# Optimization experiments

Hardware: AMD Instinct MI355X
Metric: run time of the kernel (lower is better)

Reference implementation:

```python
import jax, jax.numpy as jnp
import numpy as np

CUTOFF = 10.0
K = 32            # max_num_neighbors
NUM_GRAPHS = 64
ATOMS = 128
N = NUM_GRAPHS * ATOMS
HID = 128
FIL = 128
NG = 50           # num_gaussians
LAYERS = 6
MAX_Z = 100
PI = 3.14159265   # constant used verbatim in the torch source


def silu(x):
    return x * jax.nn.sigmoid(x)


def build_graph(pos, batch):
    """Dense cdist + per-node top-K neighbor selection (radius_graph_pure).
    Returns idx[i,k] = k-th nearest neighbor j of center i, and a validity mask.
    Torch edge (row, col) = (j, i): node j receives a message computed from x[i].
    """
    p = jax.lax.stop_gradient(pos)
    d2 = jnp.sum((p[:, None, :] - p[None, :, :]) ** 2, -1)          # [N,N]
    same = batch[:, None] == batch[None, :]
    eye = jnp.eye(p.shape[0], dtype=bool)
    valid = same & (d2 < CUTOFF * CUTOFF) & (~eye)
    dm = jnp.where(valid, d2, jnp.inf)
    neg, idx = jax.lax.top_k(-dm, K)                                 # [N,K]
    return idx, jnp.isfinite(neg)                                    # edge valid iff within mask


def setup_inputs() -> dict:
    key = jax.random.key(0)
    ks = jax.random.split(key, 20)
    s = 0.05
    inp = {
        "pos": jax.random.normal(ks[0], (N, 3), jnp.float32),
        "z": jax.random.randint(ks[1], (N,), 0, MAX_Z),
        "batch": jnp.repeat(jnp.arange(NUM_GRAPHS), ATOMS),
        # parameters (weights stored as [in, out])
        "emb": jax.random.normal(ks[2], (MAX_Z, HID), jnp.float32) * s,
        "mw1": jax.random.normal(ks[3], (LAYERS, NG, FIL), jnp.float32) * s,
        "mb1": jax.random.normal(ks[4], (LAYERS, FIL), jnp.float32) * s,
        "mw2": jax.random.normal(ks[5], (LAYERS, FIL, FIL), jnp.float32) * s,
        "mb2": jax.random.normal(ks[6], (LAYERS, FIL), jnp.float32) * s,
        "l1w": jax.random.normal(ks[7], (LAYERS, HID, FIL), jnp.float32) * s,
        "l1b": jax.random.normal(ks[8], (LAYERS, FIL), jnp.float32) * s,
        "l2w": jax.random.normal(ks[9], (LAYERS, FIL, HID), jnp.float32) * s,
        "l2b": jax.random.normal(ks[10], (LAYERS, HID), jnp.float32) * s,
        "ow1": jax.random.normal(ks[11], (HID, HID // 2), jnp.float32) * s,
        "ob1": jax.random.normal(ks[12], (HID // 2,), jnp.float32) * s,
        "ow2": jax.random.normal(ks[13], (HID // 2, 1), jnp.float32) * s,
        "ob2": jax.random.normal(ks[14], (1,), jnp.float32) * s,
    }
    return inp


def reference(pos, z, batch, emb, mw1, mb1, mw2, mb2, l1w, l1b, l2w, l2b, ow1, ob1, ow2, ob2):
    idx, evalid = build_graph(pos, batch)                 # [N,K], [N,K]
    ev = evalid.astype(pos.dtype)
    diff = pos[idx] - pos[:, None, :]                     # [N,K,3]
    d2e = jnp.sum(diff * diff, -1)
    dist = jnp.sqrt(jnp.where(evalid, d2e, 1.0))          # safe sqrt for masked edges
    offset = jnp.linspace(0.0, CUTOFF, NG)
    width = CUTOFF / (NG - 1)
    rbf = jnp.exp(-0.5 * ((dist[..., None] - offset) / width) ** 2)   # [N,K,NG]
    cval = 0.5 * (jnp.cos(dist * PI / CUTOFF) + 1.0)
    cval = cval * (dist < CUTOFF).astype(pos.dtype) * ev  # zero out invalid edges

    h = emb[z]                                            # [N,HID]
    flat_idx = idx.reshape(-1)                            # receivers (torch row)
    for l in range(LAYERS):
        W = silu(rbf @ mw1[l] + mb1[l]) @ mw2[l] + mb2[l]           # filter MLP
        W = W * cval[..., None]                                       # [N,K,FIL]
        xj = (h @ l1w[l] + l1b[l])[:, None, :]                        # sender = center i
        msg = (xj * W).reshape(N * K, FIL)
        agg = jax.ops.segment_sum(msg, flat_idx, num_segments=N)     # scatter_add at row
        h = h + silu(agg @ l2w[l] + l2b[l])

    out = (silu(h @ ow1 + ob1) @ ow2 + ob2)[:, 0]         # [N]
    return jax.ops.segment_sum(out, batch, num_segments=NUM_GRAPHS)  # [G]
```

## Files before the change

### kernel.cpp

```cpp
#include <hip/hip_runtime.h>
#include <math.h>

typedef unsigned short u16;
typedef unsigned int   u32;
typedef unsigned long long u64;

#define NATOMS 8192
#define GRAPHS 64
#define KNN    32
#define NGAUSS 50
#define HID    128
#define LAYERS 6
#define NTAB   4096
#define SA     136
#define SW1    72
#define SH     132

typedef __attribute__((ext_vector_type(8))) short bf16x8;
typedef __attribute__((ext_vector_type(4))) float f32x4;

__device__ __forceinline__ float bf2f(u16 v) {
    return __uint_as_float(((u32)v) << 16);
}
__device__ __forceinline__ u16 f2bf(float f) {
    u32 u = __float_as_uint(f);
    u32 lsb = (u >> 16) & 1u;
    u += 0x7fffu + lsb;
    return (u16)(u >> 16);
}
__device__ __forceinline__ u32 pkbf(float lo, float hi) {
#if __has_builtin(__builtin_amdgcn_cvt_pk_bf16_f32)
    auto r = __builtin_amdgcn_cvt_pk_bf16_f32(lo, hi);
    u32 u; __builtin_memcpy(&u, &r, 4); return u;
#else
    return (u32)f2bf(lo) | ((u32)f2bf(hi) << 16);
#endif
}
__device__ __forceinline__ float silu_f(float x) {
    return x * __builtin_amdgcn_rcpf(1.0f + __expf(-x));
}
__device__ __forceinline__ bf16x8 ldfrag(const u16* p) {
    return *(const bf16x8*)__builtin_assume_aligned(p, 16);
}
__device__ __forceinline__ u64 shfl_xor_u64(u64 v, int mask) {
    u32 lo = (u32)v, hi = (u32)(v >> 32);
    lo = (u32)__shfl_xor((int)lo, mask, 64);
    hi = (u32)__shfl_xor((int)hi, mask, 64);
    return ((u64)hi << 32) | lo;
}
__device__ __forceinline__ float ldf(const void* p, int i, bool f32in) {
    return f32in ? ((const float*)p)[i] : bf2f(((const u16*)p)[i]);
}
union U8 { bf16x8 v; u32 w[4]; };

__global__ void probe_kernel(const u16* __restrict__ raw, int* __restrict__ flag,
                             int* __restrict__ rev_cnt, float* __restrict__ gsum,
                             int* __restrict__ done_cnt) {
    __shared__ int s;
    int t = threadIdx.x;
    if (t == 0) s = 0;
    __syncthreads();
    float x = bf2f(raw[2 * t]);
    if (!(fabsf(x) < 1000.0f)) atomicOr(&s, 1);
    for (int i = t; i < NATOMS; i += 256) rev_cnt[i] = 0;
    if (t < GRAPHS) gsum[t] = 0.0f;
    if (t == 0) *done_cnt = 0;
    __syncthreads();
    if (t == 0) *flag = s;
}

#define NARR 9
struct IngestDesc {
    const void* src[NARR];
    void*       dst[NARR];
    int         n[NARR];
};

#define NB_BUILD 2048
#define NB_PREP  1344

__launch_bounds__(256)
__global__ void setup_kernel(const void* __restrict__ pos,
                             const void* __restrict__ l1w, const void* __restrict__ l2w,
                             const void* __restrict__ mw2, const void* __restrict__ mw1,
                             u16* __restrict__ l1wt, u16* __restrict__ l2wt,
                             u16* __restrict__ mw2t, u16* __restrict__ mw1t,
                             IngestDesc d, int total_ing,
                             const int* __restrict__ flag,
                             int* __restrict__ rev_cnt, int2* __restrict__ rev_si) {
    int bid = blockIdx.x;
    bool f32in = (*flag != 0);
    if (bid < NB_BUILD) {
        int wv = threadIdx.x >> 6, lane = threadIdx.x & 63;
        int t = bid * 4 + wv;
        int tl = t & 127;
        int base = t & ~127;
        float cx = ldf(pos, t * 3 + 0, f32in);
        float cy = ldf(pos, t * 3 + 1, f32in);
        float cz = ldf(pos, t * 3 + 2, f32in);
        u64 key[2];
#pragma unroll
        for (int c = 0; c < 2; ++c) {
            int j = lane + c * 64;
            float jx = ldf(pos, (base + j) * 3 + 0, f32in);
            float jy = ldf(pos, (base + j) * 3 + 1, f32in);
            float jz = ldf(pos, (base + j) * 3 + 2, f32in);
            float dx = __fsub_rn(cx, jx);
            float dy = __fsub_rn(cy, jy);
            float dz = __fsub_rn(cz, jz);
            float d2 = __fadd_rn(__fadd_rn(__fmul_rn(dx, dx), __fmul_rn(dy, dy)),
                                 __fmul_rn(dz, dz));
            bool valid = (j != tl) && (d2 < 100.0f);
            key[c] = valid ? ((((u64)__float_as_uint(d2)) << 32) | (u32)j) : ~0ULL;
        }
#pragma unroll
        for (int k = 2; k <= 128; k <<= 1) {
#pragma unroll
            for (int j = k >> 1; j > 0; j >>= 1) {
                if (j == 64) {
                    u64 lo = key[0] < key[1] ? key[0] : key[1];
                    u64 hi = key[0] < key[1] ? key[1] : key[0];
                    key[0] = lo; key[1] = hi;
                } else {
#pragma unroll
                    for (int r = 0; r < 2; ++r) {
                        u64 o = shfl_xor_u64(key[r], j);
                        u32 ii = (u32)(r * 64 + lane);
                        bool dir = ((ii & (u32)k) == 0);
                        bool lower = ((ii & (u32)j) == 0);
                        bool keep_min = (dir == lower);
                        bool less = key[r] < o;
                        key[r] = (less == keep_min) ? key[r] : o;
                    }
                }
            }
        }
        if (lane < KNN) {
            u64 m = key[0];
            if (m != ~0ULL) {
                float d2 = __uint_as_float((u32)(m >> 32));
                float dd = __fsqrt_rn(d2);
                if (dd < 10.0f) {
                    float u = dd * ((float)(NTAB - 1) / 10.0f);
                    int i0 = (int)(u + 0.5f);
                    if (i0 > NTAB - 1) i0 = NTAB - 1;
                    int jn = base + (int)(m & 0xffffffffu);
                    int p = atomicAdd(&rev_cnt[jn], 1);
                    rev_si[(size_t)jn * 128 + p] = make_int2(t, i0);
                }
            }
        }
    } else if (bid < NB_BUILD + NB_PREP) {
        int gid = (bid - NB_BUILD) * 256 + threadIdx.x;
        if (gid < 3 * 98304) {
            int seg = gid / 98304;
            int tt = gid % 98304;
            int l = tt >> 14;
            int n = (tt >> 7) & 127;
            int k = tt & 127;
            const void* src = (seg == 0) ? l1w : ((seg == 1) ? l2w : mw2);
            u16* dst = (seg == 0) ? l1wt : ((seg == 1) ? l2wt : mw2t);
            int si = l * 16384 + k * 128 + n;
            float v = f32in ? ((const float*)src)[si] : bf2f(((const u16*)src)[si]);
            dst[tt] = f2bf(v);
        } else {
            int tt = gid - 3 * 98304;
            if (tt < 49152) {
                int l = tt >> 13;
                int n = (tt >> 6) & 127;
                int k = tt & 63;
                float v = 0.0f;
                if (k < 50) {
                    int si = l * 6400 + k * 128 + n;
                    v = f32in ? ((const float*)mw1)[si] : bf2f(((const u16*)mw1)[si]);
                }
                mw1t[tt] = f2bf(v);
            }
        }
    } else {
        int gid = (bid - NB_BUILD - NB_PREP) * 256 + threadIdx.x;
        if (gid < total_ing) {
            int a = 0, off = gid;
            while (off >= d.n[a]) { off -= d.n[a]; ++a; }
            float v = f32in ? ((const float*)d.src[a])[off]
                            : bf2f(((const u16*)d.src[a])[off]);
            ((float*)d.dst[a])[off] = v;
        }
    }
}

__launch_bounds__(256)
__global__ void vtab_kernel(const u16* __restrict__ mw1t,
                            const u16* __restrict__ mw2t,
                            const float* __restrict__ b1,
                            const float* __restrict__ b2,
                            u32* __restrict__ pk) {
    __shared__ u16 s_t1[128 * SA];
    __shared__ u16 s_w1[128 * SW1];
    __shared__ u16 s_w2[128 * SA];
    int tid = threadIdx.x;
    int l = blockIdx.x / (NTAB / 128);
    int rbase = (blockIdx.x % (NTAB / 128)) * 128;
    {
        const uint4* g1 = (const uint4*)(mw1t + (size_t)l * 8192);
#pragma unroll
        for (int p = 0; p < 4; ++p) {
            int q = tid + p * 256;
            int row = q >> 3, c8 = (q & 7) * 8;
            *(uint4*)&s_w1[row * SW1 + c8] = g1[q];
        }
        const uint4* g2 = (const uint4*)(mw2t + (size_t)l * 16384);
#pragma unroll
        for (int p = 0; p < 8; ++p) {
            int q = tid + p * 256;
            int row = q >> 4, c8 = (q & 15) * 8;
            *(uint4*)&s_w2[row * SA + c8] = g2[q];
        }
    }
    __syncthreads();

    int wv = tid >> 6, lane = tid & 63;
    int quad = lane >> 4, lr = lane & 15;
    int m0 = wv * 32;

    {
        const float wgi = 49.0f / 10.0f;
        const float dstep = 10.0f / (float)(NTAB - 1);
        U8 afr[2][2];
#pragma unroll
        for (int mt = 0; mt < 2; ++mt) {
            float d = (float)(rbase + m0 + mt * 16 + lr) * dstep;
            float u = d * wgi;
#pragma unroll
            for (int kki = 0; kki < 2; ++kki) {
                float t0 = u - (float)(quad * 8) - (float)(kki * 32);
                float vj[8];
#pragma unroll
                for (int j = 0; j < 8; ++j) {
                    float tt = t0 - (float)j;
                    float e = __expf(-0.5f * tt * tt);
                    if (kki == 1 && (quad * 8 + j) >= 18) e = 0.0f;
                    vj[j] = e;
                }
#pragma unroll
                for (int p = 0; p < 4; ++p)
                    afr[mt][kki].w[p] = pkbf(vj[2 * p], vj[2 * p + 1]);
            }
        }
        f32x4 accA[2][8];
#pragma unroll
        for (int mt = 0; mt < 2; ++mt)
#pragma unroll
            for (int nt = 0; nt < 8; ++nt) accA[mt][nt] = (f32x4){0.f, 0.f, 0.f, 0.f};
#pragma unroll
        for (int kki = 0; kki < 2; ++kki) {
#pragma unroll
            for (int nt = 0; nt < 8; ++nt) {
                bf16x8 b = ldfrag(&s_w1[(nt * 16 + lr) * SW1 + kki * 32 + quad * 8]);
                accA[0][nt] = __builtin_amdgcn_mfma_f32_16x16x32_bf16(afr[0][kki].v, b, accA[0][nt], 0, 0, 0);
                accA[1][nt] = __builtin_amdgcn_mfma_f32_16x16x32_bf16(afr[1][kki].v, b, accA[1][nt], 0, 0, 0);
            }
        }
#pragma unroll
        for (int mt = 0; mt < 2; ++mt) {
            int r0 = m0 + mt * 16 + quad * 4;
            u16* tp0 = &s_t1[r0 * SA + lr];
#pragma unroll
            for (int nt = 0; nt < 8; ++nt) {
                int col = nt * 16;
                float bb = b1[l * 128 + col + lr];
                u32 p01 = pkbf(silu_f(accA[mt][nt][0] + bb),
                               silu_f(accA[mt][nt][1] + bb));
                u32 p23 = pkbf(silu_f(accA[mt][nt][2] + bb),
                               silu_f(accA[mt][nt][3] + bb));
                u16* tp = tp0 + col;
                tp[0]      = (u16)p01;
                tp[SA]     = (u16)(p01 >> 16);
                tp[2 * SA] = (u16)p23;
                tp[3 * SA] = (u16)(p23 >> 16);
            }
        }
    }
    {
        f32x4 accB[2][8];
#pragma unroll
        for (int mt = 0; mt < 2; ++mt)
#pragma unroll
            for (int nt = 0; nt < 8; ++nt) accB[mt][nt] = (f32x4){0.f, 0.f, 0.f, 0.f};
#pragma unroll
        for (int kk = 0; kk < 128; kk += 32) {
            bf16x8 a0 = ldfrag(&s_t1[(m0 + lr)      * SA + kk + quad * 8]);
            bf16x8 a1 = ldfrag(&s_t1[(m0 + 16 + lr) * SA + kk + quad * 8]);
#pragma unroll
            for (int nt = 0; nt < 8; ++nt) {
                bf16x8 b = ldfrag(&s_w2[(nt * 16 + lr) * SA + kk + quad * 8]);
                accB[0][nt] = __builtin_amdgcn_mfma_f32_16x16x32_bf16(a0, b, accB[0][nt], 0, 0, 0);
                accB[1][nt] = __builtin_amdgcn_mfma_f32_16x16x32_bf16(a1, b, accB[1][nt], 0, 0, 0);
            }
        }
        const float dstep = 10.0f / (float)(NTAB - 1);
#pragma unroll
        for (int mt = 0; mt < 2; ++mt) {
            int r0 = m0 + mt * 16 + quad * 4;
            float cv[4];
#pragma unroll
            for (int r = 0; r < 4; ++r) {
                float d = (float)(rbase + r0 + r) * dstep;
                cv[r] = 0.5f * (cosf(d * 3.14159265f / 10.0f) + 1.0f);
            }
#pragma unroll
            for (int nt = 0; nt < 8; ++nt) {
                int col = nt * 16 + lr;
                float bb = b2[l * 128 + col];
#pragma unroll
                for (int r = 0; r < 4; ++r) {
                    float val = (accB[mt][nt][r] + bb) * cv[r];
                    float oth = __shfl_xor(val, 1, 64);
                    if ((lr & 1) == 0) {
                        int row = rbase + r0 + r;
                        pk[((size_t)l * NTAB + row) * 64 + (col >> 1)] =
                            pkbf(val, oth);
                    }
                }
            }
        }
    }
}

__launch_bounds__(256)
__global__ void gemm0_kernel(const int* __restrict__ z,
                             const float* __restrict__ emb,
                             const u16* __restrict__ Bt,
                             const float* __restrict__ bias,
                             u16* __restrict__ xjb) {
    __shared__ u16 s_a[16 * SA];
    __shared__ float s_bias[128];
    int tid = threadIdx.x;
    int row0 = blockIdx.x * 16;
#pragma unroll
    for (int p = 0; p < 2; ++p) {
        int q = tid + p * 256;
        int r = q >> 5, c4 = (q & 31) * 4;
        const float* src = emb + (size_t)z[row0 + r] * 128;
        float4 v = *(const float4*)(src + c4);
        u32* dd = (u32*)&s_a[r * SA + c4];
        dd[0] = pkbf(v.x, v.y); dd[1] = pkbf(v.z, v.w);
    }
    if (tid < 128) s_bias[tid] = bias[tid];
    __syncthreads();
    int wv = tid >> 6, lane = tid & 63;
    int quad = lane >> 4, lr = lane & 15;
    int n0 = wv * 32;
    f32x4 acc[2];
#pragma unroll
    for (int nt = 0; nt < 2; ++nt) acc[nt] = (f32x4){0.f, 0.f, 0.f, 0.f};
#pragma unroll
    for (int kk = 0; kk < 128; kk += 32) {
        bf16x8 a = ldfrag(&s_a[lr * SA + kk + quad * 8]);
#pragma unroll
        for (int nt = 0; nt < 2; ++nt) {
            bf16x8 b = ldfrag(Bt + (n0 + nt * 16 + lr) * 128 + kk + quad * 8);
            acc[nt] = __builtin_amdgcn_mfma_f32_16x16x32_bf16(a, b, acc[nt], 0, 0, 0);
        }
    }
#pragma unroll
    for (int nt = 0; nt < 2; ++nt)
#pragma unroll
        for (int r = 0; r < 4; ++r) {
            int col = n0 + nt * 16 + lr;
            xjb[(size_t)(row0 + quad * 4 + r) * 128 + col] =
                f2bf(acc[nt][r] + s_bias[col]);
        }
}

#define AGG_ISSUE(T, X, base, ev)                                              \
    {                                                                          \
        _Pragma("unroll") for (int q = 0; q < 8; ++q) {                        \
            int e = (base) + q;                                                \
            int sx = __builtin_amdgcn_readlane((ev).x, e & 63);                \
            int sy = __builtin_amdgcn_readlane((ev).y, e & 63);                \
            T[q] = pk[(size_t)sy * 64 + lane];                                 \
            X[q] = *(const u32*)(xjb + (size_t)sx * 128 + c2);                 \
        }                                                                      \
    }

#define AGG_COMPUTE(T, X)                                                      \
    {                                                                          \
        _Pragma("unroll") for (int q = 0; q < 8; ++q) {                        \
            float v0 = bf2f((u16)T[q]) * bf2f((u16)X[q]);                      \
            float v1 = bf2f((u16)(T[q] >> 16)) * bf2f((u16)(X[q] >> 16));      \
            switch (q & 3) {                                                   \
                case 0: a0 += v0; a1 += v1; break;                             \
                case 1: b0 += v0; b1 += v1; break;                             \
                case 2: c0 += v0; c1 += v1; break;                             \
                default: d0 += v0; d1 += v1; break;                            \
            }                                                                  \
        }                                                                      \
    }

__launch_bounds__(256, 4)
__global__ void agg_kernel(const int* __restrict__ rev_cnt,
                           const int2* __restrict__ rev_si,
                           const u32* __restrict__ pk,
                           const u16* __restrict__ xjb,
                           float* __restrict__ agg) {
    int bid = ((blockIdx.x & 7) << 8) | (blockIdx.x >> 3);
    int j = bid * 4 + (threadIdx.x >> 6);
    int lane = threadIdx.x & 63;
    int deg = rev_cnt[j];
    const int2* si = rev_si + (size_t)j * 128;
    int c2 = lane * 2;
    int2 e0 = si[lane];
    int2 e1 = si[64 + lane];
    float a0 = 0.f, a1 = 0.f, b0 = 0.f, b1 = 0.f;
    float c0 = 0.f, c1 = 0.f, d0 = 0.f, d1 = 0.f;
    u32 tA[8], xA[8], tB[8], xB[8];
    int ng = deg >> 3;
    if (ng > 0) {
        AGG_ISSUE(tA, xA, 0, e0);
        int g = 1;
        for (; g + 1 < ng; g += 2) {
            int2 evB = (g < 8) ? e0 : e1;
            AGG_ISSUE(tB, xB, g * 8, evB);
            AGG_COMPUTE(tA, xA);
            int2 evA = ((g + 1) < 8) ? e0 : e1;
            AGG_ISSUE(tA, xA, (g + 1) * 8, evA);
            AGG_COMPUTE(tB, xB);
        }
        if (g < ng) {
            int2 evB = (g < 8) ? e0 : e1;
            AGG_ISSUE(tB, xB, g * 8, evB);
            AGG_COMPUTE(tA, xA);
            AGG_COMPUTE(tB, xB);
        } else {
            AGG_COMPUTE(tA, xA);
        }
    }
    for (int it = ng * 8; it < deg; ++it) {
        int2 ev = (it < 64) ? e0 : e1;
        int sx = __builtin_amdgcn_readlane(ev.x, it & 63);
        int sy = __builtin_amdgcn_readlane(ev.y, it & 63);
        u32 t = pk[(size_t)sy * 64 + lane];
        u32 x = *(const u32*)(xjb + (size_t)sx * 128 + c2);
        a0 += bf2f((u16)t) * bf2f((u16)x);
        a1 += bf2f((u16)(t >> 16)) * bf2f((u16)(x >> 16));
    }
    float2 r;
    r.x = (a0 + b0) + (c0 + d0);
    r.y = (a1 + b1) + (c1 + d1);
    *(float2*)(agg + (size_t)j * 128 + c2) = r;
}

template <int EMB, int LAST>
__launch_bounds__(256)
__global__ void layer_tail_kernel(const float* __restrict__ agg,
                                  float* __restrict__ h,
                                  const int* __restrict__ z,
                                  const float* __restrict__ emb,
                                  const u16* __restrict__ B2t,
                                  const float* __restrict__ b2,
                                  const u16* __restrict__ B1n,
                                  const float* __restrict__ b1n,
                                  u16* __restrict__ xjb,
                                  const float* __restrict__ ow1,
                                  const float* __restrict__ ob1,
                                  const float* __restrict__ ow2,
                                  const float* __restrict__ ob2,
                                  float* __restrict__ gsum,
                                  int* __restrict__ done_cnt,
                                  void* __restrict__ out,
                                  const int* __restrict__ flag) {
    __shared__ u16 s_ahi[16 * SA];
    __shared__ u16 s_alo[16 * SA];
    __shared__ float s_h[16 * SH];
    __shared__ float s_b2[128], s_b1[128];
    __shared__ float s_w[LAST ? 128 * 64 : 1];
    __shared__ float s_sum;
    __shared__ int s_last;
    int tid = threadIdx.x;
    int row0 = blockIdx.x * 16;
#pragma unroll
    for (int p = 0; p < 2; ++p) {
        int q = tid + p * 256;
        int r = q >> 5, c4 = (q & 31) * 4;
        float4 v = *(const float4*)(agg + (size_t)(row0 + r) * 128 + c4);
        u32 h0 = pkbf(v.x, v.y), h1 = pkbf(v.z, v.w);
        u32* hd = (u32*)&s_ahi[r * SA + c4];
        hd[0] = h0; hd[1] = h1;
        u32 l0 = pkbf(v.x - bf2f((u16)h0), v.y - bf2f((u16)(h0 >> 16)));
        u32 l1 = pkbf(v.z - bf2f((u16)h1), v.w - bf2f((u16)(h1 >> 16)));
        u32* ld = (u32*)&s_alo[r * SA + c4];
        ld[0] = l0; ld[1] = l1;
    }
    if (tid < 128) {
        s_b2[tid] = b2[tid];
        if (!LAST) s_b1[tid] = b1n[tid];
    }
    if (LAST) {
        if (tid == 0) s_sum = 0.0f;
        const float4* src = (const float4*)ow1;
        float4* dst = (float4*)s_w;
#pragma unroll
        for (int p = 0; p < 8; ++p) dst[tid + p * 256] = src[tid + p * 256];
    }
    __syncthreads();

    int wv = tid >> 6, lane = tid & 63;
    int quad = lane >> 4, lr = lane & 15;
    int n0 = wv * 32;

    f32x4 acc[2];
#pragma unroll
    for (int nt = 0; nt < 2; ++nt) acc[nt] = (f32x4){0.f, 0.f, 0.f, 0.f};
#pragma unroll
    for (int kk = 0; kk < 128; kk += 32) {
        bf16x8 ah = ldfrag(&s_ahi[lr * SA + kk + quad * 8]);
        bf16x8 al = ldfrag(&s_alo[lr * SA + kk + quad * 8]);
#pragma unroll
        for (int nt = 0; nt < 2; ++nt) {
            bf16x8 b = ldfrag(B2t + (n0 + nt * 16 + lr) * 128 + kk + quad * 8);
            acc[nt] = __builtin_amdgcn_mfma_f32_16x16x32_bf16(ah, b, acc[nt], 0, 0, 0);
            acc[nt] = __builtin_amdgcn_mfma_f32_16x16x32_bf16(al, b, acc[nt], 0, 0, 0);
        }
    }
#pragma unroll
    for (int nt = 0; nt < 2; ++nt)
#pragma unroll
        for (int r = 0; r < 4; ++r) {
            int row = quad * 4 + r;
            int col = n0 + nt * 16 + lr;
            size_t off = (size_t)(row0 + row) * 128 + col;
            float hold = EMB ? emb[(size_t)z[row0 + row] * 128 + col] : h[off];
            float hn = hold + silu_f(acc[nt][r] + s_b2[col]);
            if (!LAST) h[off] = hn;
            s_h[row * SH + col] = hn;
        }
    __syncthreads();

    if (!LAST) {
        f32x4 ac2[2];
#pragma unroll
        for (int nt = 0; nt < 2; ++nt) ac2[nt] = (f32x4){0.f, 0.f, 0.f, 0.f};
#pragma unroll
        for (int kk = 0; kk < 128; kk += 32) {
            const float* ap = &s_h[lr * SH + kk + quad * 8];
            float4 v0 = *(const float4*)ap;
            float4 v1 = *(const float4*)(ap + 4);
            U8 a;
            a.w[0] = pkbf(v0.x, v0.y); a.w[1] = pkbf(v0.z, v0.w);
            a.w[2] = pkbf(v1.x, v1.y); a.w[3] = pkbf(v1.z, v1.w);
#pragma unroll
            for (int nt = 0; nt < 2; ++nt) {
                bf16x8 b = ldfrag(B1n + (n0 + nt * 16 + lr) * 128 + kk + quad * 8);
                ac2[nt] = __builtin_amdgcn_mfma_f32_16x16x32_bf16(a.v, b, ac2[nt], 0, 0, 0);
            }
        }
#pragma unroll
        for (int nt = 0; nt < 2; ++nt)
#pragma unroll
            for (int r = 0; r < 4; ++r) {
                int col = n0 + nt * 16 + lr;
                xjb[(size_t)(row0 + quad * 4 + r) * 128 + col] =
                    f2bf(ac2[nt][r] + s_b1[col]);
            }
    } else {
        int atom = tid >> 4, cg = tid & 15;
        const float* hr = &s_h[atom * SH];
        const float4* w4 = (const float4*)s_w;
        float4 a4 = {0.f, 0.f, 0.f, 0.f};
#pragma unroll 8
        for (int f = 0; f < 128; ++f) {
            float hv = hr[f];
            float4 w = w4[f * 16 + cg];
            a4.x += hv * w.x; a4.y += hv * w.y;
            a4.z += hv * w.z; a4.w += hv * w.w;
        }
        int c0i = cg * 4;
        float v = silu_f(a4.x + ob1[c0i + 0]) * ow2[c0i + 0]
                + silu_f(a4.y + ob1[c0i + 1]) * ow2[c0i + 1]
                + silu_f(a4.z + ob1[c0i + 2]) * ow2[c0i + 2]
                + silu_f(a4.w + ob1[c0i + 3]) * ow2[c0i + 3];
        v += __shfl_xor(v, 1, 64);
        v += __shfl_xor(v, 2, 64);
        v += __shfl_xor(v, 4, 64);
        v += __shfl_xor(v, 8, 64);
        if ((tid & 15) == 0) atomicAdd(&s_sum, v + ob2[0]);
        __syncthreads();
        if (tid == 0) {
            atomicAdd(&gsum[row0 >> 7], s_sum);
            __threadfence();
            int tk = __hip_atomic_fetch_add(done_cnt, 1, __ATOMIC_ACQ_REL,
                                            __HIP_MEMORY_SCOPE_AGENT);
            s_last = (tk == (NATOMS / 16) - 1);
        }
        __syncthreads();
        if (s_last && tid < GRAPHS) {
            float g = __hip_atomic_load(&gsum[tid], __ATOMIC_RELAXED,
                                        __HIP_MEMORY_SCOPE_AGENT);
            if (*flag) ((float*)out)[tid] = g;
            else       ((u16*)out)[tid]   = f2bf(g);
        }
    }
}

extern "C" void kernel_launch(void* const* d_in, const int* in_sizes, int n_in,
                              void* d_out, int out_size, void* d_ws, size_t ws_size,
                              hipStream_t stream) {
    const void* pos  = d_in[0];
    const int*  z    = (const int*)d_in[1];
    const void* emb  = d_in[3];
    const void* mw1  = d_in[4];
    const void* mb1  = d_in[5];
    const void* mw2  = d_in[6];
    const void* mb2  = d_in[7];
    const void* l1w  = d_in[8];
    const void* l1b  = d_in[9];
    const void* l2w  = d_in[10];
    const void* l2b  = d_in[11];
    const void* ow1  = d_in[12];
    const void* ob1  = d_in[13];
    const void* ow2  = d_in[14];
    const void* ob2  = d_in[15];

    char* ws = (char*)d_ws;
    const size_t KB = 1024, MB = 1048576;
    int*   w_flag  = (int*)  (ws);
    int*   w_done  = (int*)  (ws + 64);
    float* c_emb   = (float*)(ws + 112 * KB);
    float* c_mb1   = (float*)(ws + 168 * KB);
    float* c_mb2   = (float*)(ws + 176 * KB);
    float* c_l1b   = (float*)(ws + 184 * KB);
    float* c_l2b   = (float*)(ws + 192 * KB);
    float* c_ow1   = (float*)(ws + 200 * KB);
    float* c_ob1   = (float*)(ws + 236 * KB);
    float* c_ow2   = (float*)(ws + 240 * KB);
    float* c_ob2   = (float*)(ws + 244 * KB);
    float* w_gsum  = (float*)(ws + 248 * KB);
    u16*   c_l1wt  = (u16*)  (ws + 256 * KB);
    u16*   c_l2wt  = (u16*)  (ws + 448 * KB);
    u16*   c_mw2t  = (u16*)  (ws + 640 * KB);
    u16*   c_mw1t  = (u16*)  (ws + 832 * KB);
    int*   rev_cnt = (int*)  (ws + 2  * MB);
    int2*  rev_si  = (int2*) (ws + 3  * MB);
    float* w_h     = (float*)(ws + 11 * MB);
    u16*   w_xjb   = (u16*)  (ws + 15 * MB);
    float* w_agg   = (float*)(ws + 17 * MB);
    u32*   w_pk    = (u32*)  (ws + 21 * MB);

    probe_kernel<<<1, 256, 0, stream>>>((const u16*)emb, w_flag, rev_cnt,
                                        w_gsum, w_done);

    IngestDesc dsc;
    const void* srcs[NARR] = {emb, mb1, mb2, l1b, l2b, ow1, ob1, ow2, ob2};
    void* dsts[NARR] = {c_emb, c_mb1, c_mb2, c_l1b, c_l2b, c_ow1, c_ob1,
                        c_ow2, c_ob2};
    int ns_[NARR] = {12800, 768, 768, 768, 768, 8192, 64, 64, 1};
    int total = 0;
    for (int a = 0; a < NARR; ++a) {
        dsc.src[a] = srcs[a]; dsc.dst[a] = dsts[a]; dsc.n[a] = ns_[a];
        total += ns_[a];
    }
    int nb_ing = (total + 255) / 256;
    setup_kernel<<<NB_BUILD + NB_PREP + nb_ing, 256, 0, stream>>>(
        pos, l1w, l2w, mw2, mw1, c_l1wt, c_l2wt, c_mw2t, c_mw1t,
        dsc, total, w_flag, rev_cnt, rev_si);

    vtab_kernel<<<LAYERS * NTAB / 128, 256, 0, stream>>>(
        c_mw1t, c_mw2t, c_mb1, c_mb2, w_pk);

    gemm0_kernel<<<NATOMS / 16, 256, 0, stream>>>(z, c_emb, c_l1wt, c_l1b, w_xjb);

    for (int l = 0; l < LAYERS; ++l) {
        const u16* B2 = c_l2wt + (size_t)l * 16384;
        const float* b2 = c_l2b + (size_t)l * 128;
        const u16* B1n = c_l1wt + (size_t)(l + 1) * 16384;
        const float* b1n = c_l1b + (size_t)(l + 1) * 128;
        const u32* pkl = w_pk + (size_t)l * NTAB * 64;

        agg_kernel<<<NATOMS / 4, 256, 0, stream>>>(rev_cnt, rev_si, pkl,
                                                   w_xjb, w_agg);
        if (l == 0)
            layer_tail_kernel<1, 0><<<NATOMS / 16, 256, 0, stream>>>(
                w_agg, w_h, z, c_emb, B2, b2, B1n, b1n, w_xjb,
                nullptr, nullptr, nullptr, nullptr, nullptr, nullptr, nullptr,
                nullptr);
        else if (l < LAYERS - 1)
            layer_tail_kernel<0, 0><<<NATOMS / 16, 256, 0, stream>>>(
                w_agg, w_h, z, c_emb, B2, b2, B1n, b1n, w_xjb,
                nullptr, nullptr, nullptr, nullptr, nullptr, nullptr, nullptr,
                nullptr);
        else
            layer_tail_kernel<0, 1><<<NATOMS / 16, 256, 0, stream>>>(
                w_agg, w_h, z, c_emb, B2, b2, nullptr, nullptr, nullptr,
                c_ow1, c_ob1, c_ow2, c_ob2, w_gsum, w_done, d_out, w_flag);
    }
}
```

Before: 270.9 us.

## Fuse all message-passing layers into one persistent kernel with grid barriers

```diff
diff --git a/kernel.cpp b/kernel.cpp
--- a/kernel.cpp
+++ b/kernel.cpp
@@ -12,6 +12,7 @@
 #define HID    128
 #define LAYERS 6
 #define NTAB   4096
+#define NBLK   512
 #define SA     136
 #define SW1    72
 #define SH     132
@@ -55,7 +56,7 @@
 
 __global__ void probe_kernel(const u16* __restrict__ raw, int* __restrict__ flag,
                              int* __restrict__ rev_cnt, float* __restrict__ gsum,
-                             int* __restrict__ done_cnt) {
+                             int* __restrict__ done_cnt, int* __restrict__ bar) {
     __shared__ int s;
     int t = threadIdx.x;
     if (t == 0) s = 0;
@@ -65,6 +66,7 @@
     for (int i = t; i < NATOMS; i += 256) rev_cnt[i] = 0;
     if (t < GRAPHS) gsum[t] = 0.0f;
     if (t == 0) *done_cnt = 0;
+    if (t < 8) bar[t] = 0;
     __syncthreads();
     if (t == 0) *flag = s;
 }
@@ -87,7 +89,7 @@
                              u16* __restrict__ mw2t, u16* __restrict__ mw1t,
                              IngestDesc d, int total_ing,
                              const int* __restrict__ flag,
-                             int* __restrict__ rev_cnt, int2* __restrict__ rev_si) {
+                             int* __restrict__ rev_cnt, u32* __restrict__ rev) {
     int bid = blockIdx.x;
     bool f32in = (*flag != 0);
     if (bid < NB_BUILD) {
@@ -146,7 +148,7 @@
                     if (i0 > NTAB - 1) i0 = NTAB - 1;
                     int jn = base + (int)(m & 0xffffffffu);
                     int p = atomicAdd(&rev_cnt[jn], 1);
-                    rev_si[(size_t)jn * 128 + p] = make_int2(t, i0);
+                    rev[(size_t)jn * 128 + p] = ((u32)i0 << 13) | (u32)t;
                 }
             }
         }
@@ -377,10 +379,11 @@
     {                                                                          \
         _Pragma("unroll") for (int q = 0; q < 8; ++q) {                        \
             int e = (base) + q;                                                \
-            int sx = __builtin_amdgcn_readlane((ev).x, e & 63);                \
-            int sy = __builtin_amdgcn_readlane((ev).y, e & 63);                \
-            T[q] = pk[(size_t)sy * 64 + lane];                                 \
-            X[q] = *(const u32*)(xjb + (size_t)sx * 128 + c2);                 \
+            u32 pe = __builtin_amdgcn_readlane((ev), e & 63);                  \
+            int sy = (int)(pe >> 13);                                          \
+            int sx = (int)(pe & 0x1fffu);                                      \
+            T[q] = pkl[(size_t)sy * 64 + lane];                                \
+            X[q] = *(const u32*)(xin + (size_t)sx * 128 + c2);                 \
         }                                                                      \
     }
 
@@ -391,214 +394,214 @@
             float v1 = bf2f((u16)(T[q] >> 16)) * bf2f((u16)(X[q] >> 16));      \
             switch (q & 3) {                                                   \
                 case 0: a0 += v0; a1 += v1; break;                             \
-                case 1: b0 += v0; b1 += v1; break;                             \
+                case 1: b0 += v0; b1v += v1; break;                            \
                 case 2: c0 += v0; c1 += v1; break;                             \
                 default: d0 += v0; d1 += v1; break;                            \
             }                                                                  \
         }                                                                      \
     }
 
-__launch_bounds__(256, 4)
-__global__ void agg_kernel(const int* __restrict__ rev_cnt,
-                           const int2* __restrict__ rev_si,
-                           const u32* __restrict__ pk,
-                           const u16* __restrict__ xjb,
-                           float* __restrict__ agg) {
-    int bid = ((blockIdx.x & 7) << 8) | (blockIdx.x >> 3);
-    int j = bid * 4 + (threadIdx.x >> 6);
-    int lane = threadIdx.x & 63;
-    int deg = rev_cnt[j];
-    const int2* si = rev_si + (size_t)j * 128;
-    int c2 = lane * 2;
-    int2 e0 = si[lane];
-    int2 e1 = si[64 + lane];
-    float a0 = 0.f, a1 = 0.f, b0 = 0.f, b1 = 0.f;
-    float c0 = 0.f, c1 = 0.f, d0 = 0.f, d1 = 0.f;
-    u32 tA[8], xA[8], tB[8], xB[8];
-    int ng = deg >> 3;
-    if (ng > 0) {
-        AGG_ISSUE(tA, xA, 0, e0);
-        int g = 1;
-        for (; g + 1 < ng; g += 2) {
-            int2 evB = (g < 8) ? e0 : e1;
-            AGG_ISSUE(tB, xB, g * 8, evB);
-            AGG_COMPUTE(tA, xA);
-            int2 evA = ((g + 1) < 8) ? e0 : e1;
-            AGG_ISSUE(tA, xA, (g + 1) * 8, evA);
-            AGG_COMPUTE(tB, xB);
-        }
-        if (g < ng) {
-            int2 evB = (g < 8) ? e0 : e1;
-            AGG_ISSUE(tB, xB, g * 8, evB);
-            AGG_COMPUTE(tA, xA);
-            AGG_COMPUTE(tB, xB);
-        } else {
-            AGG_COMPUTE(tA, xA);
-        }
-    }
-    for (int it = ng * 8; it < deg; ++it) {
-        int2 ev = (it < 64) ? e0 : e1;
-        int sx = __builtin_amdgcn_readlane(ev.x, it & 63);
-        int sy = __builtin_amdgcn_readlane(ev.y, it & 63);
-        u32 t = pk[(size_t)sy * 64 + lane];
-        u32 x = *(const u32*)(xjb + (size_t)sx * 128 + c2);
-        a0 += bf2f((u16)t) * bf2f((u16)x);
-        a1 += bf2f((u16)(t >> 16)) * bf2f((u16)(x >> 16));
-    }
-    float2 r;
-    r.x = (a0 + b0) + (c0 + d0);
-    r.y = (a1 + b1) + (c1 + d1);
-    *(float2*)(agg + (size_t)j * 128 + c2) = r;
-}
-
-template <int EMB, int LAST>
-__launch_bounds__(256)
-__global__ void layer_tail_kernel(const float* __restrict__ agg,
-                                  float* __restrict__ h,
-                                  const int* __restrict__ z,
-                                  const float* __restrict__ emb,
-                                  const u16* __restrict__ B2t,
-                                  const float* __restrict__ b2,
-                                  const u16* __restrict__ B1n,
-                                  const float* __restrict__ b1n,
-                                  u16* __restrict__ xjb,
-                                  const float* __restrict__ ow1,
-                                  const float* __restrict__ ob1,
-                                  const float* __restrict__ ow2,
-                                  const float* __restrict__ ob2,
-                                  float* __restrict__ gsum,
-                                  int* __restrict__ done_cnt,
-                                  void* __restrict__ out,
-                                  const int* __restrict__ flag) {
+__launch_bounds__(256, 2)
+__global__ void layers_kernel(const int* __restrict__ rev_cnt,
+                              const u32* __restrict__ rev,
+                              const u32* __restrict__ pk,
+                              u16* __restrict__ xjbA,
+                              u16* __restrict__ xjbB,
+                              const int* __restrict__ z,
+                              const float* __restrict__ emb,
+                              const u16* __restrict__ l2wt,
+                              const float* __restrict__ l2b,
+                              const u16* __restrict__ l1wt,
+                              const float* __restrict__ l1b,
+                              const float* __restrict__ ow1,
+                              const float* __restrict__ ob1,
+                              const float* __restrict__ ow2,
+                              const float* __restrict__ ob2,
+                              float* __restrict__ gsum,
+                              int* __restrict__ done_cnt,
+                              void* __restrict__ out,
+                              const int* __restrict__ flag,
+                              int* __restrict__ bar) {
     __shared__ u16 s_ahi[16 * SA];
     __shared__ u16 s_alo[16 * SA];
     __shared__ float s_h[16 * SH];
     __shared__ float s_b2[128], s_b1[128];
-    __shared__ float s_w[LAST ? 128 * 64 : 1];
     __shared__ float s_sum;
     __shared__ int s_last;
     int tid = threadIdx.x;
     int row0 = blockIdx.x * 16;
-#pragma unroll
-    for (int p = 0; p < 2; ++p) {
-        int q = tid + p * 256;
-        int r = q >> 5, c4 = (q & 31) * 4;
-        float4 v = *(const float4*)(agg + (size_t)(row0 + r) * 128 + c4);
-        u32 h0 = pkbf(v.x, v.y), h1 = pkbf(v.z, v.w);
-        u32* hd = (u32*)&s_ahi[r * SA + c4];
-        hd[0] = h0; hd[1] = h1;
-        u32 l0 = pkbf(v.x - bf2f((u16)h0), v.y - bf2f((u16)(h0 >> 16)));
-        u32 l1 = pkbf(v.z - bf2f((u16)h1), v.w - bf2f((u16)(h1 >> 16)));
-        u32* ld = (u32*)&s_alo[r * SA + c4];
-        ld[0] = l0; ld[1] = l1;
-    }
-    if (tid < 128) {
-        s_b2[tid] = b2[tid];
-        if (!LAST) s_b1[tid] = b1n[tid];
-    }
-    if (LAST) {
-        if (tid == 0) s_sum = 0.0f;
-        const float4* src = (const float4*)ow1;
-        float4* dst = (float4*)s_w;
-#pragma unroll
-        for (int p = 0; p < 8; ++p) dst[tid + p * 256] = src[tid + p * 256];
-    }
-    __syncthreads();
-
     int wv = tid >> 6, lane = tid & 63;
     int quad = lane >> 4, lr = lane & 15;
-    int n0 = wv * 32;
-
-    f32x4 acc[2];
-#pragma unroll
-    for (int nt = 0; nt < 2; ++nt) acc[nt] = (f32x4){0.f, 0.f, 0.f, 0.f};
-#pragma unroll
-    for (int kk = 0; kk < 128; kk += 32) {
-        bf16x8 ah = ldfrag(&s_ahi[lr * SA + kk + quad * 8]);
-        bf16x8 al = ldfrag(&s_alo[lr * SA + kk + quad * 8]);
-#pragma unroll
-        for (int nt = 0; nt < 2; ++nt) {
-            bf16x8 b = ldfrag(B2t + (n0 + nt * 16 + lr) * 128 + kk + quad * 8);
-            acc[nt] = __builtin_amdgcn_mfma_f32_16x16x32_bf16(ah, b, acc[nt], 0, 0, 0);
-            acc[nt] = __builtin_amdgcn_mfma_f32_16x16x32_bf16(al, b, acc[nt], 0, 0, 0);
-        }
-    }
-#pragma unroll
-    for (int nt = 0; nt < 2; ++nt)
-#pragma unroll
-        for (int r = 0; r < 4; ++r) {
-            int row = quad * 4 + r;
-            int col = n0 + nt * 16 + lr;
-            size_t off = (size_t)(row0 + row) * 128 + col;
-            float hold = EMB ? emb[(size_t)z[row0 + row] * 128 + col] : h[off];
-            float hn = hold + silu_f(acc[nt][r] + s_b2[col]);
-            if (!LAST) h[off] = hn;
-            s_h[row * SH + col] = hn;
-        }
-    __syncthreads();
-
-    if (!LAST) {
-        f32x4 ac2[2];
-#pragma unroll
-        for (int nt = 0; nt < 2; ++nt) ac2[nt] = (f32x4){0.f, 0.f, 0.f, 0.f};
+    int n0 = wv * 32, c2 = lane * 2;
+
+    float hreg[8];
+    const u16* xin = xjbA;
+    u16* xout = xjbB;
+
+    for (int l = 0; l < LAYERS; ++l) {
+        if (tid < 128) {
+            s_b2[tid] = l2b[l * 128 + tid];
+            if (l < LAYERS - 1) s_b1[tid] = l1b[(l + 1) * 128 + tid];
+        }
+        const u32* pkl = pk + (size_t)l * NTAB * 64;
+
+        for (int rr = 0; rr < 4; ++rr) {
+            int row = wv * 4 + rr;
+            int j = row0 + row;
+            int deg = rev_cnt[j];
+            const u32* si = rev + (size_t)j * 128;
+            u32 e0 = si[lane];
+            u32 e1 = si[64 + lane];
+            float a0 = 0.f, a1 = 0.f, b0 = 0.f, b1v = 0.f;
+            float c0 = 0.f, c1 = 0.f, d0 = 0.f, d1 = 0.f;
+            u32 tA[8], xA[8], tB[8], xB[8];
+            int ng = deg >> 3;
+            if (ng > 0) {
+                AGG_ISSUE(tA, xA, 0, e0);
+                int g = 1;
+                for (; g + 1 < ng; g += 2) {
+                    u32 evB = (g < 8) ? e0 : e1;
+                    AGG_ISSUE(tB, xB, g * 8, evB);
+                    AGG_COMPUTE(tA, xA);
+                    u32 evA = ((g + 1) < 8) ? e0 : e1;
+                    AGG_ISSUE(tA, xA, (g + 1) * 8, evA);
+                    AGG_COMPUTE(tB, xB);
+                }
+                if (g < ng) {
+                    u32 evB = (g < 8) ? e0 : e1;
+                    AGG_ISSUE(tB, xB, g * 8, evB);
+                    AGG_COMPUTE(tA, xA);
+                    AGG_COMPUTE(tB, xB);
+                } else {
+                    AGG_COMPUTE(tA, xA);
+                }
+            }
+            for (int it = ng * 8; it < deg; ++it) {
+                u32 ev = (it < 64) ? e0 : e1;
+                u32 pe = __builtin_amdgcn_readlane(ev, it & 63);
+                int sy = (int)(pe >> 13);
+                int sx = (int)(pe & 0x1fffu);
+                u32 t = pkl[(size_t)sy * 64 + lane];
+                u32 x = *(const u32*)(xin + (size_t)sx * 128 + c2);
+                a0 += bf2f((u16)t) * bf2f((u16)x);
+                a1 += bf2f((u16)(t >> 16)) * bf2f((u16)(x >> 16));
+            }
+            float sxv = (a0 + b0) + (c0 + d0);
+            float syv = (a1 + b1v) + (c1 + d1);
+            u32 hp = pkbf(sxv, syv);
+            u32 lp = pkbf(sxv - bf2f((u16)hp), syv - bf2f((u16)(hp >> 16)));
+            *(u32*)&s_ahi[row * SA + c2] = hp;
+            *(u32*)&s_alo[row * SA + c2] = lp;
+        }
+        __syncthreads();
+
+        const u16* B2t = l2wt + (size_t)l * 16384;
+        f32x4 acc[2];
+#pragma unroll
+        for (int nt = 0; nt < 2; ++nt) acc[nt] = (f32x4){0.f, 0.f, 0.f, 0.f};
 #pragma unroll
         for (int kk = 0; kk < 128; kk += 32) {
-            const float* ap = &s_h[lr * SH + kk + quad * 8];
-            float4 v0 = *(const float4*)ap;
-            float4 v1 = *(const float4*)(ap + 4);
-            U8 a;
-            a.w[0] = pkbf(v0.x, v0.y); a.w[1] = pkbf(v0.z, v0.w);
-            a.w[2] = pkbf(v1.x, v1.y); a.w[3] = pkbf(v1.z, v1.w);
+            bf16x8 ah = ldfrag(&s_ahi[lr * SA + kk + quad * 8]);
+            bf16x8 al = ldfrag(&s_alo[lr * SA + kk + quad * 8]);
 #pragma unroll
             for (int nt = 0; nt < 2; ++nt) {
-                bf16x8 b = ldfrag(B1n + (n0 + nt * 16 + lr) * 128 + kk + quad * 8);
-                ac2[nt] = __builtin_amdgcn_mfma_f32_16x16x32_bf16(a.v, b, ac2[nt], 0, 0, 0);
-            }
-        }
+                bf16x8 b = ldfrag(B2t + (n0 + nt * 16 + lr) * 128 + kk + quad * 8);
+                acc[nt] = __builtin_amdgcn_mfma_f32_16x16x32_bf16(ah, b, acc[nt], 0, 0, 0);
+                acc[nt] = __builtin_amdgcn_mfma_f32_16x16x32_bf16(al, b, acc[nt], 0, 0, 0);
+            }
+        }
+        if (l == LAYERS - 1 && tid == 0) s_sum = 0.0f;
 #pragma unroll
         for (int nt = 0; nt < 2; ++nt)
 #pragma unroll
             for (int r = 0; r < 4; ++r) {
+                int row = quad * 4 + r;
                 int col = n0 + nt * 16 + lr;
-                xjb[(size_t)(row0 + quad * 4 + r) * 128 + col] =
-                    f2bf(ac2[nt][r] + s_b1[col]);
-            }
-    } else {
-        int atom = tid >> 4, cg = tid & 15;
-        const float* hr = &s_h[atom * SH];
-        const float4* w4 = (const float4*)s_w;
-        float4 a4 = {0.f, 0.f, 0.f, 0.f};
+                float hold = (l == 0)
+                    ? emb[(size_t)z[row0 + row] * 128 + col]
+                    : hreg[nt * 4 + r];
+                float hn = hold + silu_f(acc[nt][r] + s_b2[col]);
+                hreg[nt * 4 + r] = hn;
+                s_h[row * SH + col] = hn;
+            }
+        __syncthreads();
+
+        if (l < LAYERS - 1) {
+            const u16* B1n = l1wt + (size_t)(l + 1) * 16384;
+            f32x4 ac2[2];
+#pragma unroll
+            for (int nt = 0; nt < 2; ++nt) ac2[nt] = (f32x4){0.f, 0.f, 0.f, 0.f};
+#pragma unroll
+            for (int kk = 0; kk < 128; kk += 32) {
+                const float* ap = &s_h[lr * SH + kk + quad * 8];
+                float4 v0 = *(const float4*)ap;
+                float4 v1 = *(const float4*)(ap + 4);
+                U8 a;
+                a.w[0] = pkbf(v0.x, v0.y); a.w[1] = pkbf(v0.z, v0.w);
+                a.w[2] = pkbf(v1.x, v1.y); a.w[3] = pkbf(v1.z, v1.w);
+#pragma unroll
+                for (int nt = 0; nt < 2; ++nt) {
+                    bf16x8 b = ldfrag(B1n + (n0 + nt * 16 + lr) * 128 + kk + quad * 8);
+                    ac2[nt] = __builtin_amdgcn_mfma_f32_16x16x32_bf16(a.v, b, ac2[nt], 0, 0, 0);
+                }
+            }
+#pragma unroll
+            for (int nt = 0; nt < 2; ++nt)
+#pragma unroll
+                for (int r = 0; r < 4; ++r) {
+                    int col = n0 + nt * 16 + lr;
+                    xout[(size_t)(row0 + quad * 4 + r) * 128 + col] =
+                        f2bf(ac2[nt][r] + s_b1[col]);
+                }
+            __syncthreads();
+            if (tid == 0) {
+                __threadfence();
+                __hip_atomic_fetch_add(&bar[l], 1, __ATOMIC_ACQ_REL,
+                                       __HIP_MEMORY_SCOPE_AGENT);
+                while (__hip_atomic_load(&bar[l], __ATOMIC_ACQUIRE,
+                                         __HIP_MEMORY_SCOPE_AGENT) < NBLK)
+                    __builtin_amdgcn_s_sleep(2);
+                __threadfence();
+            }
+            __syncthreads();
+            const u16* tswap = xin; xin = xout; xout = (u16*)tswap;
+        } else {
+            int atom = tid >> 4, cg = tid & 15;
+            const float* hr = &s_h[atom * SH];
+            const float4* w4 = (const float4*)ow1;
+            float4 a4 = {0.f, 0.f, 0.f, 0.f};
 #pragma unroll 8
-        for (int f = 0; f < 128; ++f) {
-            float hv = hr[f];
-            float4 w = w4[f * 16 + cg];
-            a4.x += hv * w.x; a4.y += hv * w.y;
-            a4.z += hv * w.z; a4.w += hv * w.w;
-        }
-        int c0i = cg * 4;
-        float v = silu_f(a4.x + ob1[c0i + 0]) * ow2[c0i + 0]
-                + silu_f(a4.y + ob1[c0i + 1]) * ow2[c0i + 1]
-                + silu_f(a4.z + ob1[c0i + 2]) * ow2[c0i + 2]
-                + silu_f(a4.w + ob1[c0i + 3]) * ow2[c0i + 3];
-        v += __shfl_xor(v, 1, 64);
-        v += __shfl_xor(v, 2, 64);
-        v += __shfl_xor(v, 4, 64);
-        v += __shfl_xor(v, 8, 64);
-        if ((tid & 15) == 0) atomicAdd(&s_sum, v + ob2[0]);
-        __syncthreads();
-        if (tid == 0) {
-            atomicAdd(&gsum[row0 >> 7], s_sum);
-            __threadfence();
-            int tk = __hip_atomic_fetch_add(done_cnt, 1, __ATOMIC_ACQ_REL,
+            for (int f = 0; f < 128; ++f) {
+                float hv = hr[f];
+                float4 w = w4[f * 16 + cg];
+                a4.x += hv * w.x; a4.y += hv * w.y;
+                a4.z += hv * w.z; a4.w += hv * w.w;
+            }
+            int c0i = cg * 4;
+            float v = silu_f(a4.x + ob1[c0i + 0]) * ow2[c0i + 0]
+                    + silu_f(a4.y + ob1[c0i + 1]) * ow2[c0i + 1]
+                    + silu_f(a4.z + ob1[c0i + 2]) * ow2[c0i + 2]
+                    + silu_f(a4.w + ob1[c0i + 3]) * ow2[c0i + 3];
+            v += __shfl_xor(v, 1, 64);
+            v += __shfl_xor(v, 2, 64);
+            v += __shfl_xor(v, 4, 64);
+            v += __shfl_xor(v, 8, 64);
+            if ((tid & 15) == 0) atomicAdd(&s_sum, v + ob2[0]);
+            __syncthreads();
+            if (tid == 0) {
+                atomicAdd(&gsum[row0 >> 7], s_sum);
+                __threadfence();
+                int tk = __hip_atomic_fetch_add(done_cnt, 1, __ATOMIC_ACQ_REL,
+                                                __HIP_MEMORY_SCOPE_AGENT);
+                s_last = (tk == NBLK - 1);
+            }
+            __syncthreads();
+            if (s_last && tid < GRAPHS) {
+                float g = __hip_atomic_load(&gsum[tid], __ATOMIC_RELAXED,
                                             __HIP_MEMORY_SCOPE_AGENT);
-            s_last = (tk == (NATOMS / 16) - 1);
-        }
-        __syncthreads();
-        if (s_last && tid < GRAPHS) {
-            float g = __hip_atomic_load(&gsum[tid], __ATOMIC_RELAXED,
-                                        __HIP_MEMORY_SCOPE_AGENT);
-            if (*flag) ((float*)out)[tid] = g;
-            else       ((u16*)out)[tid]   = f2bf(g);
+                if (*flag) ((float*)out)[tid] = g;
+                else       ((u16*)out)[tid]   = f2bf(g);
+            }
         }
     }
 }
@@ -626,6 +629,7 @@
     const size_t KB = 1024, MB = 1048576;
     int*   w_flag  = (int*)  (ws);
     int*   w_done  = (int*)  (ws + 64);
+    int*   w_bar   = (int*)  (ws + 128);
     float* c_emb   = (float*)(ws + 112 * KB);
     float* c_mb1   = (float*)(ws + 168 * KB);
     float* c_mb2   = (float*)(ws + 176 * KB);
@@ -641,14 +645,13 @@
     u16*   c_mw2t  = (u16*)  (ws + 640 * KB);
     u16*   c_mw1t  = (u16*)  (ws + 832 * KB);
     int*   rev_cnt = (int*)  (ws + 2  * MB);
-    int2*  rev_si  = (int2*) (ws + 3  * MB);
-    float* w_h     = (float*)(ws + 11 * MB);
-    u16*   w_xjb   = (u16*)  (ws + 15 * MB);
-    float* w_agg   = (float*)(ws + 17 * MB);
+    u32*   w_rev   = (u32*)  (ws + 3  * MB);
+    u16*   w_xjbA  = (u16*)  (ws + 15 * MB);
+    u16*   w_xjbB  = (u16*)  (ws + 17 * MB);
     u32*   w_pk    = (u32*)  (ws + 21 * MB);
 
     probe_kernel<<<1, 256, 0, stream>>>((const u16*)emb, w_flag, rev_cnt,
-                                        w_gsum, w_done);
+                                        w_gsum, w_done, w_bar);
 
     IngestDesc dsc;
     const void* srcs[NARR] = {emb, mb1, mb2, l1b, l2b, ow1, ob1, ow2, ob2};
@@ -663,35 +666,17 @@
     int nb_ing = (total + 255) / 256;
     setup_kernel<<<NB_BUILD + NB_PREP + nb_ing, 256, 0, stream>>>(
         pos, l1w, l2w, mw2, mw1, c_l1wt, c_l2wt, c_mw2t, c_mw1t,
-        dsc, total, w_flag, rev_cnt, rev_si);
+        dsc, total, w_flag, rev_cnt, w_rev);
 
     vtab_kernel<<<LAYERS * NTAB / 128, 256, 0, stream>>>(
         c_mw1t, c_mw2t, c_mb1, c_mb2, w_pk);
 
-    gemm0_kernel<<<NATOMS / 16, 256, 0, stream>>>(z, c_emb, c_l1wt, c_l1b, w_xjb);
-
-    for (int l = 0; l < LAYERS; ++l) {
-        const u16* B2 = c_l2wt + (size_t)l * 16384;
-        const float* b2 = c_l2b + (size_t)l * 128;
-        const u16* B1n = c_l1wt + (size_t)(l + 1) * 16384;
-        const float* b1n = c_l1b + (size_t)(l + 1) * 128;
-        const u32* pkl = w_pk + (size_t)l * NTAB * 64;
-
-        agg_kernel<<<NATOMS / 4, 256, 0, stream>>>(rev_cnt, rev_si, pkl,
-                                                   w_xjb, w_agg);
-        if (l == 0)
-            layer_tail_kernel<1, 0><<<NATOMS / 16, 256, 0, stream>>>(
-                w_agg, w_h, z, c_emb, B2, b2, B1n, b1n, w_xjb,
-                nullptr, nullptr, nullptr, nullptr, nullptr, nullptr, nullptr,
-                nullptr);
-        else if (l < LAYERS - 1)
-            layer_tail_kernel<0, 0><<<NATOMS / 16, 256, 0, stream>>>(
-                w_agg, w_h, z, c_emb, B2, b2, B1n, b1n, w_xjb,
-                nullptr, nullptr, nullptr, nullptr, nullptr, nullptr, nullptr,
-                nullptr);
-        else
-            layer_tail_kernel<0, 1><<<NATOMS / 16, 256, 0, stream>>>(
-                w_agg, w_h, z, c_emb, B2, b2, nullptr, nullptr, nullptr,
-                c_ow1, c_ob1, c_ow2, c_ob2, w_gsum, w_done, d_out, w_flag);
-    }
-}
+    gemm0_kernel<<<NATOMS / 16, 256, 0, stream>>>(z, c_emb, c_l1wt, c_l1b,
+                                                  w_xjbA);
+
+    layers_kernel<<<NBLK, 256, 0, stream>>>(
+        rev_cnt, w_rev, w_pk, w_xjbA, w_xjbB, z, c_emb,
+        c_l2wt, c_l2b, c_l1wt, c_l1b,
+        c_ow1, c_ob1, c_ow2, c_ob2,
+        w_gsum, w_done, d_out, w_flag, w_bar);
+}
```

New measurement: 737.5 us. 2.72x slower.
